# Performance work log

Hardware: AMD Instinct MI355X
Metric: run time of the kernel (lower is better)

## Reference

```python
import jax, jax.numpy as jnp
import numpy as np

E = 8       # num experts
D = 768     # embed_dim
H = 12      # num heads
F = 3072    # expert hidden = 4*D
TOPK = 2


def setup_inputs() -> dict:
    key = jax.random.key(0)
    ks = jax.random.split(key, 8)
    B, S = 4, 1024
    s = lambda d: 1.0 / np.sqrt(d)
    return {
        "x": jax.random.normal(ks[0], (B, S, D), jnp.float32),
        "w_qkv": jax.random.normal(ks[1], (D, 3 * D), jnp.float32) * s(D),
        "b_qkv": jnp.zeros((3 * D,), jnp.float32),
        "w_o": jax.random.normal(ks[2], (D, D), jnp.float32) * s(D),
        "b_o": jnp.zeros((D,), jnp.float32),
        "w_router": jax.random.normal(ks[3], (D, E), jnp.float32) * s(D),
        "w1": jax.random.normal(ks[4], (E, D, F), jnp.float32) * s(D),
        "b1": jnp.zeros((E, F), jnp.float32),
        "w2": jax.random.normal(ks[5], (E, F, D), jnp.float32) * s(F),
        "b2": jnp.zeros((E, D), jnp.float32),
    }


def reference(x, w_qkv, b_qkv, w_o, b_o, w_router, w1, b1, w2, b2):
    B, S, Dm = x.shape
    hd = Dm // H
    # --- multi-head self-attention ---
    qkv = x @ w_qkv + b_qkv                                  # [B,S,3D]
    q, k, v = jnp.split(qkv, 3, axis=-1)
    resh = lambda t: t.reshape(B, S, H, hd).transpose(0, 2, 1, 3)  # [B,H,S,hd]
    q, k, v = resh(q), resh(k), resh(v)
    scores = jnp.einsum('bhqd,bhkd->bhqk', q, k) / np.sqrt(hd).astype(np.float32)
    attn = jax.nn.softmax(scores, axis=-1)
    ctx = jnp.einsum('bhqk,bhkd->bhqd', attn, v)
    ctx = ctx.transpose(0, 2, 1, 3).reshape(B, S, Dm)
    y = ctx @ w_o + b_o                                      # [B,S,D]
    # --- top-k MoE feed-forward ---
    t = y.reshape(B * S, Dm)                                 # [T,D]
    logits = t @ w_router                                    # [T,E]
    probs = jax.nn.softmax(logits, axis=-1)
    topv, topi = jax.lax.top_k(probs, TOPK)                  # [T,K]
    topw = topv / jnp.sum(topv, axis=-1, keepdims=True)      # renormalized gates
    T = t.shape[0]
    wfull = jnp.zeros_like(probs).at[jnp.arange(T)[:, None], topi].set(topw)  # [T,E]
    # dense all-expert compute, weighted combine (faithful to routed math)
    h = jax.nn.gelu(jnp.einsum('td,edf->etf', t, w1) + b1[:, None, :])  # [E,T,F]
    oe = jnp.einsum('etf,efd->etd', h, w2) + b2[:, None, :]              # [E,T,D]
    out = jnp.einsum('te,etd->td', wfull, oe).reshape(B, S, Dm)
    diagnostics = probs  # router probabilities as diagnostics
    return (out, diagnostics)
```

## Files before the change

kernel.cpp:

```cpp
#include <hip/hip_runtime.h>
#include <hip/hip_bf16.h>
#include <cstdint>
#include <cmath>

#define T_TOK 4096
#define DIM   768
#define HEADS 12
#define HD    64
#define NEXP  8
#define FDIM  3072

typedef __attribute__((ext_vector_type(8))) short short8v;
typedef __attribute__((ext_vector_type(4))) float float4v;

__device__ __forceinline__ float gelu_tanh(float x) {
  float u = 0.7978845608028654f * (x + 0.044715f * x * x * x);
  return 0.5f * x * (1.0f + tanhf(u));
}

__device__ __forceinline__ short f2bf(float x) {
  __hip_bfloat16 h = __float2bfloat16(x);
  return *reinterpret_cast<short*>(&h);
}

template<int TBM, int TBN>
__global__ __launch_bounds__(256) void gemm_f32(
    const float* __restrict__ A, const float* __restrict__ W,
    const float* __restrict__ bias, float* __restrict__ C,
    int M, int N, int K)
{
  constexpr int MM = TBM / 16;
  constexpr int MN = TBN / 16;
  constexpr int ALOAD = TBM * 16 / 256;
  constexpr int BLOAD = TBN * 16 / 256;
  __shared__ float As[16][TBM + 4];
  __shared__ float Bs[16][TBN + 4];
  const int bm = blockIdx.y * TBM;
  const int bn = blockIdx.x * TBN;
  const int tid = threadIdx.x;
  const int tr = tid >> 4;
  const int tc = tid & 15;

  float acc[MM][MN] = {};

  for (int k0 = 0; k0 < K; k0 += 16) {
    #pragma unroll
    for (int i = 0; i < ALOAD; i++) {
      int idx = tid + i * 256;
      int m  = idx >> 4;
      int kk = idx & 15;
      As[kk][m] = A[(size_t)(bm + m) * K + k0 + kk];
    }
    #pragma unroll
    for (int i = 0; i < BLOAD; i++) {
      int idx = tid + i * 256;
      int kk = idx / TBN;
      int n  = idx % TBN;
      Bs[kk][n] = W[(size_t)(k0 + kk) * N + bn + n];
    }
    __syncthreads();
    #pragma unroll
    for (int kk = 0; kk < 16; kk++) {
      float a[MM], b[MN];
      #pragma unroll
      for (int u4 = 0; u4 < MM / 4; u4++) {
        float4 t = *(const float4*)&As[kk][tr * MM + u4 * 4];
        a[u4*4+0]=t.x; a[u4*4+1]=t.y; a[u4*4+2]=t.z; a[u4*4+3]=t.w;
      }
      #pragma unroll
      for (int v4 = 0; v4 < MN / 4; v4++) {
        float4 t = *(const float4*)&Bs[kk][tc * MN + v4 * 4];
        b[v4*4+0]=t.x; b[v4*4+1]=t.y; b[v4*4+2]=t.z; b[v4*4+3]=t.w;
      }
      #pragma unroll
      for (int u = 0; u < MM; u++)
        #pragma unroll
        for (int v = 0; v < MN; v++)
          acc[u][v] = fmaf(a[u], b[v], acc[u][v]);
    }
    __syncthreads();
  }

  #pragma unroll
  for (int u = 0; u < MM; u++) {
    int row = bm + tr * MM + u;
    #pragma unroll
    for (int v4 = 0; v4 < MN / 4; v4++) {
      int col = bn + tc * MN + v4 * 4;
      float4 o;
      o.x = acc[u][v4*4+0] + bias[col+0];
      o.y = acc[u][v4*4+1] + bias[col+1];
      o.z = acc[u][v4*4+2] + bias[col+2];
      o.w = acc[u][v4*4+3] + bias[col+3];
      *(float4*)&C[(size_t)row * N + col] = o;
    }
  }
}

__global__ __launch_bounds__(256) void transpose_bf16(
    const float* __restrict__ W, short* __restrict__ WT, int K, int N)
{
  __shared__ float t[32][33];
  const size_t mat = (size_t)K * N;
  const float* Wp = W + blockIdx.z * mat;
  short* WTp = WT + blockIdx.z * mat;
  int n0 = blockIdx.x * 32, k0 = blockIdx.y * 32;
  int tx = threadIdx.x, ty = threadIdx.y;
  #pragma unroll
  for (int i = 0; i < 4; i++)
    t[ty + i * 8][tx] = Wp[(size_t)(k0 + ty + i * 8) * N + n0 + tx];
  __syncthreads();
  #pragma unroll
  for (int i = 0; i < 4; i++)
    WTp[(size_t)(n0 + ty + i * 8) * K + k0 + tx] = f2bf(t[tx][ty + i * 8]);
}

__global__ __launch_bounds__(256) void y2bf_kernel(
    const float* __restrict__ y, short* __restrict__ ybf)
{
  int g = blockIdx.x * 256 + threadIdx.x;
  float4 v = *(const float4*)&y[(size_t)g * 4];
  short4 s = make_short4(f2bf(v.x), f2bf(v.y), f2bf(v.z), f2bf(v.w));
  *(short4*)&ybf[(size_t)g * 4] = s;
}

__global__ __launch_bounds__(256) void moe_up(
    const short* __restrict__ ybf, const short* __restrict__ WT,
    const float* __restrict__ bias, short* __restrict__ hbuf,
    const int* __restrict__ offsets, const int* __restrict__ perm)
{
  const int e = blockIdx.z;
  const int start = offsets[e];
  const int M = offsets[e + 1] - start;
  const int bm = blockIdx.y * 128;
  if (bm >= M) return;
  const int bn = blockIdx.x * 128;

  __shared__ short As[4][128][8];
  __shared__ short Bs[4][128][8];
  __shared__ int   perm_s[128];

  const int tid  = threadIdx.x;
  const int lane = tid & 63;
  const int wave = tid >> 6;
  const int wm = wave >> 1, wn = wave & 1;
  const int lr = lane & 15;
  const int kb = lane >> 4;

  const short* WTe = WT + (size_t)e * ((size_t)FDIM * DIM);
  const float* be  = bias + (size_t)e * FDIM;

  if (tid < 128) {
    int rr = bm + tid;
    perm_s[tid] = (rr < M) ? perm[start + rr] : perm[start];
  }
  __syncthreads();

  const int q = tid & 3;
  const int mrow = tid >> 2;
  const short* aptr[2];
  const short* bptr[2];
  #pragma unroll
  for (int i = 0; i < 2; i++) {
    aptr[i] = ybf + (size_t)perm_s[mrow + i * 64] * DIM;
    bptr[i] = WTe + (size_t)(bn + mrow + i * 64) * DIM;
  }

  float4v acc[4][4] = {};

  for (int k0 = 0; k0 < DIM; k0 += 32) {
    int4 av[2], bv[2];
    #pragma unroll
    for (int i = 0; i < 2; i++) {
      av[i] = *(const int4*)(aptr[i] + k0 + q * 8);
      bv[i] = *(const int4*)(bptr[i] + k0 + q * 8);
    }
    __syncthreads();
    #pragma unroll
    for (int i = 0; i < 2; i++) {
      *(int4*)&As[q][mrow + i * 64][0] = av[i];
      *(int4*)&Bs[q][mrow + i * 64][0] = bv[i];
    }
    __syncthreads();

    short8v af[4], bfv[4];
    #pragma unroll
    for (int mi = 0; mi < 4; mi++)
      af[mi] = *(const short8v*)&As[kb][wm * 64 + mi * 16 + lr][0];
    #pragma unroll
    for (int ni = 0; ni < 4; ni++)
      bfv[ni] = *(const short8v*)&Bs[kb][wn * 64 + ni * 16 + lr][0];
    #pragma unroll
    for (int mi = 0; mi < 4; mi++)
      #pragma unroll
      for (int ni = 0; ni < 4; ni++)
        acc[mi][ni] = __builtin_amdgcn_mfma_f32_16x16x32_bf16(
            af[mi], bfv[ni], acc[mi][ni], 0, 0, 0);
  }

  #pragma unroll
  for (int ni = 0; ni < 4; ni++) {
    int col = bn + wn * 64 + ni * 16 + lr;
    float b = be[col];
    #pragma unroll
    for (int mi = 0; mi < 4; mi++) {
      int lrow0 = wm * 64 + mi * 16 + kb * 4;
      #pragma unroll
      for (int r = 0; r < 4; r++) {
        int rr = bm + lrow0 + r;
        if (rr < M)
          hbuf[(size_t)(start + rr) * FDIM + col] = f2bf(gelu_tanh(acc[mi][ni][r] + b));
      }
    }
  }
}

__global__ __launch_bounds__(256) void moe_down(
    const short* __restrict__ hbuf, const short* __restrict__ WT,
    const float* __restrict__ bias, float* __restrict__ oe,
    const int* __restrict__ offsets)
{
  const int e = blockIdx.z;
  const int start = offsets[e];
  const int M = offsets[e + 1] - start;
  const int bm = blockIdx.y * 64;
  if (bm >= M) return;
  const int bn = blockIdx.x * 128;

  __shared__ short As[4][64][8];
  __shared__ short Bs[4][128][8];

  const int tid  = threadIdx.x;
  const int lane = tid & 63;
  const int wn   = tid >> 6;
  const int lr   = lane & 15;
  const int kb   = lane >> 4;

  const short* WTe = WT + (size_t)e * ((size_t)DIM * FDIM);
  const float* be  = bias + (size_t)e * DIM;

  const int q = tid & 3;
  const int mrow = tid >> 2;
  int rr0 = bm + mrow; if (rr0 >= M) rr0 = M - 1;
  const short* aptr = hbuf + (size_t)(start + rr0) * FDIM;
  const short* bptr[2];
  #pragma unroll
  for (int i = 0; i < 2; i++)
    bptr[i] = WTe + (size_t)(bn + mrow + i * 64) * FDIM;

  float4v acc[4][2] = {};

  for (int k0 = 0; k0 < FDIM; k0 += 32) {
    int4 av = *(const int4*)(aptr + k0 + q * 8);
    int4 bv[2];
    #pragma unroll
    for (int i = 0; i < 2; i++) bv[i] = *(const int4*)(bptr[i] + k0 + q * 8);
    __syncthreads();
    *(int4*)&As[q][mrow][0] = av;
    #pragma unroll
    for (int i = 0; i < 2; i++) *(int4*)&Bs[q][mrow + i * 64][0] = bv[i];
    __syncthreads();

    short8v af[4], bfv[2];
    #pragma unroll
    for (int mi = 0; mi < 4; mi++)
      af[mi] = *(const short8v*)&As[kb][mi * 16 + lr][0];
    #pragma unroll
    for (int ni = 0; ni < 2; ni++)
      bfv[ni] = *(const short8v*)&Bs[kb][wn * 32 + ni * 16 + lr][0];
    #pragma unroll
    for (int mi = 0; mi < 4; mi++)
      #pragma unroll
      for (int ni = 0; ni < 2; ni++)
        acc[mi][ni] = __builtin_amdgcn_mfma_f32_16x16x32_bf16(
            af[mi], bfv[ni], acc[mi][ni], 0, 0, 0);
  }

  #pragma unroll
  for (int ni = 0; ni < 2; ni++) {
    int col = bn + wn * 32 + ni * 16 + lr;
    float b = be[col];
    #pragma unroll
    for (int mi = 0; mi < 4; mi++) {
      #pragma unroll
      for (int r = 0; r < 4; r++) {
        int rr = bm + mi * 16 + kb * 4 + r;
        if (rr < M)
          oe[(size_t)(start + rr) * DIM + col] = acc[mi][ni][r] + b;
      }
    }
  }
}

__global__ __launch_bounds__(256) void combine_kernel(
    const float* __restrict__ oe, const int* __restrict__ ppos,
    const float* __restrict__ topg, float* __restrict__ out)
{
  int g = blockIdx.x * 256 + threadIdx.x;
  int t = g / 192;
  int c = (g - t * 192) * 4;
  int p0 = ppos[2 * t], p1 = ppos[2 * t + 1];
  float g0 = topg[2 * t], g1 = topg[2 * t + 1];
  float4 a = *(const float4*)&oe[(size_t)p0 * DIM + c];
  float4 b = *(const float4*)&oe[(size_t)p1 * DIM + c];
  float4 o;
  o.x = g0 * a.x + g1 * b.x;
  o.y = g0 * a.y + g1 * b.y;
  o.z = g0 * a.z + g1 * b.z;
  o.w = g0 * a.w + g1 * b.w;
  *(float4*)&out[(size_t)t * DIM + c] = o;
}

__global__ __launch_bounds__(512) void attn_kernel(
    const float* __restrict__ qkv, float* __restrict__ ctx)
{
  const int qt = blockIdx.x;
  const int bh = blockIdx.y;
  const int b = bh / HEADS, h = bh % HEADS;
  const float* base = qkv + (size_t)b * 1024 * (3 * DIM) + h * 64;

  __shared__ float ks[64 * 64];
  __shared__ float vs[64 * 64];
  __shared__ float ps[64 * 64];
  __shared__ float lred[3][2][32];

  const int tid   = threadIdx.x;
  const int wv    = tid >> 6;
  const int qhalf = wv & 1;
  const int kq    = wv >> 1;
  const int lane  = tid & 63;
  const int grp   = lane >> 2;
  const int sub   = lane & 3;
  const int q0    = qhalf * 32 + grp * 2;
  const int dpart = sub * 16;

  const float qscale = 0.125f * 1.44269504088896f;
  float qA[16], qB[16], accA[16] = {}, accB[16] = {};
  float lA = 0.f, lB = 0.f;

  {
    const float* qpA = base + (size_t)(qt * 64 + q0) * (3 * DIM) + dpart;
    const float* qpB = qpA + 3 * DIM;
    #pragma unroll
    for (int d4 = 0; d4 < 4; d4++) {
      float4 ta = *(const float4*)(qpA + d4 * 4);
      float4 tb = *(const float4*)(qpB + d4 * 4);
      qA[d4*4+0]=ta.x*qscale; qA[d4*4+1]=ta.y*qscale; qA[d4*4+2]=ta.z*qscale; qA[d4*4+3]=ta.w*qscale;
      qB[d4*4+0]=tb.x*qscale; qB[d4*4+1]=tb.y*qscale; qB[d4*4+2]=tb.z*qscale; qB[d4*4+3]=tb.w*qscale;
    }
  }

  for (int kt = 0; kt < 16; kt++) {
    __syncthreads();
    #pragma unroll
    for (int i = 0; i < 2; i++) {
      int idx = tid + i * 512;
      int r = idx >> 4, c4 = idx & 15;
      const float* kp = base + (size_t)(kt * 64 + r) * (3 * DIM) + c4 * 4;
      *(float4*)&ks[r * 64 + c4 * 4] = *(const float4*)(kp + DIM);
      *(float4*)&vs[r * 64 + c4 * 4] = *(const float4*)(kp + 2 * DIM);
    }
    __syncthreads();

    #pragma unroll 2
    for (int jj = 0; jj < 16; jj++) {
      int j = kq * 16 + jj;
      float4 k0v = *(const float4*)&ks[j * 64 + dpart];
      float4 k1v = *(const float4*)&ks[j * 64 + dpart + 4];
      float4 k2v = *(const float4*)&ks[j * 64 + dpart + 8];
      float4 k3v = *(const float4*)&ks[j * 64 + dpart + 12];
      float kr[16] = {k0v.x,k0v.y,k0v.z,k0v.w, k1v.x,k1v.y,k1v.z,k1v.w,
                      k2v.x,k2v.y,k2v.z,k2v.w, k3v.x,k3v.y,k3v.z,k3v.w};
      float sA = 0.f, sB = 0.f;
      #pragma unroll
      for (int d = 0; d < 16; d++) {
        sA = fmaf(qA[d], kr[d], sA);
        sB = fmaf(qB[d], kr[d], sB);
      }
      sA += __shfl_xor(sA, 1);  sB += __shfl_xor(sB, 1);
      sA += __shfl_xor(sA, 2);  sB += __shfl_xor(sB, 2);
      float pA = exp2f(sA);
      float pB = exp2f(sB);
      lA += pA;  lB += pB;
      float4 v0v = *(const float4*)&vs[j * 64 + dpart];
      float4 v1v = *(const float4*)&vs[j * 64 + dpart + 4];
      float4 v2v = *(const float4*)&vs[j * 64 + dpart + 8];
      float4 v3v = *(const float4*)&vs[j * 64 + dpart + 12];
      float vr[16] = {v0v.x,v0v.y,v0v.z,v0v.w, v1v.x,v1v.y,v1v.z,v1v.w,
                      v2v.x,v2v.y,v2v.z,v2v.w, v3v.x,v3v.y,v3v.z,v3v.w};
      #pragma unroll
      for (int d = 0; d < 16; d++) {
        accA[d] = fmaf(pA, vr[d], accA[d]);
        accB[d] = fmaf(pB, vr[d], accB[d]);
      }
    }
  }

  __syncthreads();
  if (kq != 0) {
    float* buf = (kq == 1) ? ks : (kq == 2) ? vs : ps;
    buf += qhalf * 2048;
    #pragma unroll
    for (int d4 = 0; d4 < 4; d4++) {
      *(float4*)&buf[(grp * 2) * 64 + dpart + d4 * 4] =
          make_float4(accA[d4*4], accA[d4*4+1], accA[d4*4+2], accA[d4*4+3]);
      *(float4*)&buf[(grp * 2 + 1) * 64 + dpart + d4 * 4] =
          make_float4(accB[d4*4], accB[d4*4+1], accB[d4*4+2], accB[d4*4+3]);
    }
    if (sub == 0) {
      lred[kq - 1][qhalf][grp * 2]     = lA;
      lred[kq - 1][qhalf][grp * 2 + 1] = lB;
    }
  }
  __syncthreads();
  if (kq == 0) {
    int oA = qhalf * 2048 + (grp * 2) * 64 + dpart;
    int oB = oA + 64;
    #pragma unroll
    for (int d4 = 0; d4 < 4; d4++) {
      float4 a1 = *(const float4*)&ks[oA + d4*4];
      float4 a2 = *(const float4*)&vs[oA + d4*4];
      float4 a3 = *(const float4*)&ps[oA + d4*4];
      accA[d4*4+0] += a1.x + a2.x + a3.x;
      accA[d4*4+1] += a1.y + a2.y + a3.y;
      accA[d4*4+2] += a1.z + a2.z + a3.z;
      accA[d4*4+3] += a1.w + a2.w + a3.w;
      float4 b1 = *(const float4*)&ks[oB + d4*4];
      float4 b2 = *(const float4*)&vs[oB + d4*4];
      float4 b3 = *(const float4*)&ps[oB + d4*4];
      accB[d4*4+0] += b1.x + b2.x + b3.x;
      accB[d4*4+1] += b1.y + b2.y + b3.y;
      accB[d4*4+2] += b1.z + b2.z + b3.z;
      accB[d4*4+3] += b1.w + b2.w + b3.w;
    }
    lA += lred[0][qhalf][grp*2]   + lred[1][qhalf][grp*2]   + lred[2][qhalf][grp*2];
    lB += lred[0][qhalf][grp*2+1] + lred[1][qhalf][grp*2+1] + lred[2][qhalf][grp*2+1];
    float invA = 1.f / lA, invB = 1.f / lB;
    float* opA = ctx + ((size_t)b * 1024 + qt * 64 + q0) * DIM + h * 64 + dpart;
    float* opB = opA + DIM;
    #pragma unroll
    for (int d4 = 0; d4 < 4; d4++) {
      float4 oa, ob;
      oa.x = accA[d4*4+0]*invA; oa.y = accA[d4*4+1]*invA;
      oa.z = accA[d4*4+2]*invA; oa.w = accA[d4*4+3]*invA;
      ob.x = accB[d4*4+0]*invB; ob.y = accB[d4*4+1]*invB;
      ob.z = accB[d4*4+2]*invB; ob.w = accB[d4*4+3]*invB;
      *(float4*)(opA + d4 * 4) = oa;
      *(float4*)(opB + d4 * 4) = ob;
    }
  }
}

__global__ __launch_bounds__(256) void router_kernel(
    const float* __restrict__ y, const float* __restrict__ wr,
    float* __restrict__ probs, int* __restrict__ topi,
    float* __restrict__ topg, int* __restrict__ counts)
{
  __shared__ float w[DIM * NEXP];
  const int tid = threadIdx.x;
  for (int i = tid; i < DIM * NEXP; i += 256) w[i] = wr[i];
  __syncthreads();

  const int t = blockIdx.x * 256 + tid;
  const float* yp = y + (size_t)t * DIM;
  float logit[8] = {};
  for (int d = 0; d < DIM; d++) {
    float xv = yp[d];
    #pragma unroll
    for (int e = 0; e < 8; e++) logit[e] = fmaf(xv, w[d * 8 + e], logit[e]);
  }
  float mx = logit[0];
  #pragma unroll
  for (int e = 1; e < 8; e++) mx = fmaxf(mx, logit[e]);
  float p[8], sum = 0.f;
  #pragma unroll
  for (int e = 0; e < 8; e++) { p[e] = __expf(logit[e] - mx); sum += p[e]; }
  float inv = 1.f / sum;
  #pragma unroll
  for (int e = 0; e < 8; e++) { p[e] *= inv; probs[(size_t)t * 8 + e] = p[e]; }

  int i0 = 0;
  #pragma unroll
  for (int e = 1; e < 8; e++) if (p[e] > p[i0]) i0 = e;
  int i1 = (i0 == 0) ? 1 : 0;
  #pragma unroll
  for (int e = 0; e < 8; e++) if (e != i0 && p[e] > p[i1]) i1 = e;
  float g = p[i0] + p[i1];
  topi[2 * t] = i0;  topi[2 * t + 1] = i1;
  topg[2 * t] = p[i0] / g;  topg[2 * t + 1] = p[i1] / g;
  atomicAdd(&counts[i0], 1);
  atomicAdd(&counts[i1], 1);
}

__global__ void init_meta(int* counts) {
  if (threadIdx.x < 8) counts[threadIdx.x] = 0;
}

__global__ void scan_kernel(const int* __restrict__ counts,
                            int* __restrict__ offsets, int* __restrict__ cursors) {
  if (threadIdx.x == 0) {
    int s = 0;
    for (int e = 0; e < 8; e++) { offsets[e] = s; cursors[e] = s; s += counts[e]; }
    offsets[8] = s;
  }
}

__global__ __launch_bounds__(256) void scatter_kernel(
    const int* __restrict__ topi, int* __restrict__ cursors,
    int* __restrict__ perm, int* __restrict__ ppos)
{
  const int t = blockIdx.x * 256 + threadIdx.x;
  #pragma unroll
  for (int s = 0; s < 2; s++) {
    int e = topi[2 * t + s];
    int pos = atomicAdd(&cursors[e], 1);
    perm[pos] = t;
    ppos[2 * t + s] = pos;
  }
}

extern "C" void kernel_launch(void* const* d_in, const int* in_sizes, int n_in,
                              void* d_out, int out_size, void* d_ws, size_t ws_size,
                              hipStream_t stream) {
  const float* x        = (const float*)d_in[0];
  const float* w_qkv    = (const float*)d_in[1];
  const float* b_qkv    = (const float*)d_in[2];
  const float* w_o      = (const float*)d_in[3];
  const float* b_o      = (const float*)d_in[4];
  const float* w_router = (const float*)d_in[5];
  const float* w1       = (const float*)d_in[6];
  const float* b1       = (const float*)d_in[7];
  const float* w2       = (const float*)d_in[8];
  const float* b2       = (const float*)d_in[9];

  float* out   = (float*)d_out;
  float* probs = out + (size_t)T_TOK * DIM;

  char* ws = (char*)d_ws;
  float* qkv  = (float*)ws;
  short* hbuf = (short*)ws;
  short* wT   = (short*)(ws + 50331648);
  float* ctx  = (float*)(ws + 88080384);
  short* ybf  = (short*)(ws + 88080384);
  float* oe   = (float*)(ws + 88080384);
  float* y    = (float*)(ws + 100663296);
  char*  meta = ws + 113246208;
  int*   counts  = (int*)meta;
  int*   cursors = counts + 8;
  int*   offsets = cursors + 8;
  int*   topi    = offsets + 16;
  float* topg    = (float*)(topi + 8192);
  int*   perm    = (int*)(topg + 8192);
  int*   ppos    = perm + 8192;

  init_meta<<<1, 64, 0, stream>>>(counts);

  gemm_f32<128, 64><<<dim3((3 * DIM) / 64, T_TOK / 128), 256, 0, stream>>>(
      x, w_qkv, b_qkv, qkv, T_TOK, 3 * DIM, DIM);

  attn_kernel<<<dim3(16, 48), 512, 0, stream>>>(qkv, ctx);

  gemm_f32<64, 64><<<dim3(DIM / 64, T_TOK / 64), 256, 0, stream>>>(
      ctx, w_o, b_o, y, T_TOK, DIM, DIM);

  router_kernel<<<16, 256, 0, stream>>>(y, w_router, probs, topi, topg, counts);
  scan_kernel<<<1, 64, 0, stream>>>(counts, offsets, cursors);
  scatter_kernel<<<16, 256, 0, stream>>>(topi, cursors, perm, ppos);

  y2bf_kernel<<<(T_TOK * DIM / 4) / 256, 256, 0, stream>>>(y, ybf);

  transpose_bf16<<<dim3(FDIM / 32, DIM / 32, NEXP), dim3(32, 8), 0, stream>>>(
      w1, wT, DIM, FDIM);
  moe_up<<<dim3(FDIM / 128, T_TOK / 128, NEXP), 256, 0, stream>>>(
      ybf, wT, b1, hbuf, offsets, perm);

  transpose_bf16<<<dim3(DIM / 32, FDIM / 32, NEXP), dim3(32, 8), 0, stream>>>(
      w2, wT, FDIM, DIM);
  moe_down<<<dim3(DIM / 128, T_TOK / 64, NEXP), 256, 0, stream>>>(
      hbuf, wT, b2, oe, offsets);

  combine_kernel<<<(T_TOK * DIM / 4) / 256, 256, 0, stream>>>(oe, ppos, topg, out);
}
```

Before: 1.131 ms.

## Load MoE GEMM tiles directly to LDS and shrink attention reduction scratch

```diff
diff --git a/kernel.cpp b/kernel.cpp
--- a/kernel.cpp
+++ b/kernel.cpp
@@ -21,6 +21,13 @@
 __device__ __forceinline__ short f2bf(float x) {
   __hip_bfloat16 h = __float2bfloat16(x);
   return *reinterpret_cast<short*>(&h);
+}
+
+__device__ __forceinline__ void gld16(void* lds, const void* g) {
+  __builtin_amdgcn_global_load_lds(
+      (__attribute__((address_space(1))) void*)(uintptr_t)g,
+      (__attribute__((address_space(3))) void*)(uint32_t)(uintptr_t)lds,
+      16, 0, 0);
 }
 
 template<int TBM, int TBN>
@@ -156,31 +163,23 @@
   }
   __syncthreads();
 
-  const int q = tid & 3;
-  const int mrow = tid >> 2;
-  const short* aptr[2];
-  const short* bptr[2];
-  #pragma unroll
-  for (int i = 0; i < 2; i++) {
-    aptr[i] = ybf + (size_t)perm_s[mrow + i * 64] * DIM;
-    bptr[i] = WTe + (size_t)(bn + mrow + i * 64) * DIM;
-  }
+  const short* asrc0 = ybf + (size_t)perm_s[lane] * DIM + wave * 8;
+  const short* asrc1 = ybf + (size_t)perm_s[64 + lane] * DIM + wave * 8;
+  const short* bsrc0 = WTe + (size_t)(bn + lane) * DIM + wave * 8;
+  const short* bsrc1 = WTe + (size_t)(bn + 64 + lane) * DIM + wave * 8;
+  short* adst0 = &As[wave][0][0];
+  short* adst1 = &As[wave][64][0];
+  short* bdst0 = &Bs[wave][0][0];
+  short* bdst1 = &Bs[wave][64][0];
 
   float4v acc[4][4] = {};
 
   for (int k0 = 0; k0 < DIM; k0 += 32) {
-    int4 av[2], bv[2];
-    #pragma unroll
-    for (int i = 0; i < 2; i++) {
-      av[i] = *(const int4*)(aptr[i] + k0 + q * 8);
-      bv[i] = *(const int4*)(bptr[i] + k0 + q * 8);
-    }
-    __syncthreads();
-    #pragma unroll
-    for (int i = 0; i < 2; i++) {
-      *(int4*)&As[q][mrow + i * 64][0] = av[i];
-      *(int4*)&Bs[q][mrow + i * 64][0] = bv[i];
-    }
+    __syncthreads();
+    gld16(adst0, asrc0 + k0);
+    gld16(adst1, asrc1 + k0);
+    gld16(bdst0, bsrc0 + k0);
+    gld16(bdst1, bsrc1 + k0);
     __syncthreads();
 
     short8v af[4], bfv[4];
@@ -232,33 +231,28 @@
 
   const int tid  = threadIdx.x;
   const int lane = tid & 63;
-  const int wn   = tid >> 6;
+  const int wave = tid >> 6;
   const int lr   = lane & 15;
   const int kb   = lane >> 4;
 
   const short* WTe = WT + (size_t)e * ((size_t)DIM * FDIM);
   const float* be  = bias + (size_t)e * DIM;
 
-  const int q = tid & 3;
-  const int mrow = tid >> 2;
-  int rr0 = bm + mrow; if (rr0 >= M) rr0 = M - 1;
-  const short* aptr = hbuf + (size_t)(start + rr0) * FDIM;
-  const short* bptr[2];
-  #pragma unroll
-  for (int i = 0; i < 2; i++)
-    bptr[i] = WTe + (size_t)(bn + mrow + i * 64) * FDIM;
+  int arow = bm + lane; if (arow >= M) arow = M - 1;
+  const short* asrc  = hbuf + (size_t)(start + arow) * FDIM + wave * 8;
+  const short* bsrc0 = WTe + (size_t)(bn + lane) * FDIM + wave * 8;
+  const short* bsrc1 = WTe + (size_t)(bn + 64 + lane) * FDIM + wave * 8;
+  short* adst  = &As[wave][0][0];
+  short* bdst0 = &Bs[wave][0][0];
+  short* bdst1 = &Bs[wave][64][0];
 
   float4v acc[4][2] = {};
 
   for (int k0 = 0; k0 < FDIM; k0 += 32) {
-    int4 av = *(const int4*)(aptr + k0 + q * 8);
-    int4 bv[2];
-    #pragma unroll
-    for (int i = 0; i < 2; i++) bv[i] = *(const int4*)(bptr[i] + k0 + q * 8);
-    __syncthreads();
-    *(int4*)&As[q][mrow][0] = av;
-    #pragma unroll
-    for (int i = 0; i < 2; i++) *(int4*)&Bs[q][mrow + i * 64][0] = bv[i];
+    __syncthreads();
+    gld16(adst,  asrc  + k0);
+    gld16(bdst0, bsrc0 + k0);
+    gld16(bdst1, bsrc1 + k0);
     __syncthreads();
 
     short8v af[4], bfv[2];
@@ -267,7 +261,7 @@
       af[mi] = *(const short8v*)&As[kb][mi * 16 + lr][0];
     #pragma unroll
     for (int ni = 0; ni < 2; ni++)
-      bfv[ni] = *(const short8v*)&Bs[kb][wn * 32 + ni * 16 + lr][0];
+      bfv[ni] = *(const short8v*)&Bs[kb][wave * 32 + ni * 16 + lr][0];
     #pragma unroll
     for (int mi = 0; mi < 4; mi++)
       #pragma unroll
@@ -278,7 +272,7 @@
 
   #pragma unroll
   for (int ni = 0; ni < 2; ni++) {
-    int col = bn + wn * 32 + ni * 16 + lr;
+    int col = bn + wave * 32 + ni * 16 + lr;
     float b = be[col];
     #pragma unroll
     for (int mi = 0; mi < 4; mi++) {
@@ -321,8 +315,7 @@
 
   __shared__ float ks[64 * 64];
   __shared__ float vs[64 * 64];
-  __shared__ float ps[64 * 64];
-  __shared__ float lred[3][2][32];
+  __shared__ float lred[2][2][32];
 
   const int tid   = threadIdx.x;
   const int wv    = tid >> 6;
@@ -396,45 +389,64 @@
     }
   }
 
-  __syncthreads();
-  if (kq != 0) {
-    float* buf = (kq == 1) ? ks : (kq == 2) ? vs : ps;
-    buf += qhalf * 2048;
+  float* regA = ks + qhalf * 2048;
+  float* regB = vs + qhalf * 2048;
+  const int r0 = (grp * 2) * 64 + dpart;
+  const int r1 = r0 + 64;
+
+  __syncthreads();
+  if (kq == 2 || kq == 3) {
+    float* buf = (kq == 2) ? regA : regB;
     #pragma unroll
     for (int d4 = 0; d4 < 4; d4++) {
-      *(float4*)&buf[(grp * 2) * 64 + dpart + d4 * 4] =
+      *(float4*)&buf[r0 + d4*4] =
           make_float4(accA[d4*4], accA[d4*4+1], accA[d4*4+2], accA[d4*4+3]);
-      *(float4*)&buf[(grp * 2 + 1) * 64 + dpart + d4 * 4] =
+      *(float4*)&buf[r1 + d4*4] =
           make_float4(accB[d4*4], accB[d4*4+1], accB[d4*4+2], accB[d4*4+3]);
     }
     if (sub == 0) {
-      lred[kq - 1][qhalf][grp * 2]     = lA;
-      lred[kq - 1][qhalf][grp * 2 + 1] = lB;
+      lred[kq - 2][qhalf][grp * 2]     = lA;
+      lred[kq - 2][qhalf][grp * 2 + 1] = lB;
+    }
+  }
+  __syncthreads();
+  if (kq == 0 || kq == 1) {
+    const float* buf = (kq == 0) ? regA : regB;
+    #pragma unroll
+    for (int d4 = 0; d4 < 4; d4++) {
+      float4 a = *(const float4*)&buf[r0 + d4*4];
+      float4 c = *(const float4*)&buf[r1 + d4*4];
+      accA[d4*4+0] += a.x; accA[d4*4+1] += a.y; accA[d4*4+2] += a.z; accA[d4*4+3] += a.w;
+      accB[d4*4+0] += c.x; accB[d4*4+1] += c.y; accB[d4*4+2] += c.z; accB[d4*4+3] += c.w;
+    }
+    lA += lred[kq][qhalf][grp * 2];
+    lB += lred[kq][qhalf][grp * 2 + 1];
+  }
+  __syncthreads();
+  if (kq == 1) {
+    #pragma unroll
+    for (int d4 = 0; d4 < 4; d4++) {
+      *(float4*)&regA[r0 + d4*4] =
+          make_float4(accA[d4*4], accA[d4*4+1], accA[d4*4+2], accA[d4*4+3]);
+      *(float4*)&regA[r1 + d4*4] =
+          make_float4(accB[d4*4], accB[d4*4+1], accB[d4*4+2], accB[d4*4+3]);
+    }
+    if (sub == 0) {
+      lred[0][qhalf][grp * 2]     = lA;
+      lred[0][qhalf][grp * 2 + 1] = lB;
     }
   }
   __syncthreads();
   if (kq == 0) {
-    int oA = qhalf * 2048 + (grp * 2) * 64 + dpart;
-    int oB = oA + 64;
     #pragma unroll
     for (int d4 = 0; d4 < 4; d4++) {
-      float4 a1 = *(const float4*)&ks[oA + d4*4];
-      float4 a2 = *(const float4*)&vs[oA + d4*4];
-      float4 a3 = *(const float4*)&ps[oA + d4*4];
-      accA[d4*4+0] += a1.x + a2.x + a3.x;
-      accA[d4*4+1] += a1.y + a2.y + a3.y;
-      accA[d4*4+2] += a1.z + a2.z + a3.z;
-      accA[d4*4+3] += a1.w + a2.w + a3.w;
-      float4 b1 = *(const float4*)&ks[oB + d4*4];
-      float4 b2 = *(const float4*)&vs[oB + d4*4];
-      float4 b3 = *(const float4*)&ps[oB + d4*4];
-      accB[d4*4+0] += b1.x + b2.x + b3.x;
-      accB[d4*4+1] += b1.y + b2.y + b3.y;
-      accB[d4*4+2] += b1.z + b2.z + b3.z;
-      accB[d4*4+3] += b1.w + b2.w + b3.w;
-    }
-    lA += lred[0][qhalf][grp*2]   + lred[1][qhalf][grp*2]   + lred[2][qhalf][grp*2];
-    lB += lred[0][qhalf][grp*2+1] + lred[1][qhalf][grp*2+1] + lred[2][qhalf][grp*2+1];
+      float4 a = *(const float4*)&regA[r0 + d4*4];
+      float4 c = *(const float4*)&regA[r1 + d4*4];
+      accA[d4*4+0] += a.x; accA[d4*4+1] += a.y; accA[d4*4+2] += a.z; accA[d4*4+3] += a.w;
+      accB[d4*4+0] += c.x; accB[d4*4+1] += c.y; accB[d4*4+2] += c.z; accB[d4*4+3] += c.w;
+    }
+    lA += lred[0][qhalf][grp * 2];
+    lB += lred[0][qhalf][grp * 2 + 1];
     float invA = 1.f / lA, invB = 1.f / lB;
     float* opA = ctx + ((size_t)b * 1024 + qt * 64 + q0) * DIM + h * 64 + dpart;
     float* opB = opA + DIM;
```

After: 1.080 ms. 1.05x faster.
